# Optimization experiments

Hardware: AMD Instinct MI355X
Metric: run time of the kernel (lower is better)

## Reference

```python
import jax, jax.numpy as jnp
import numpy as np
from jax import lax

B, HS, WS, C, NH, WIN = 32, 56, 56, 192, 6, 7
HID = int(C * 4.0)
EPS = 1e-5


def _ln(x, g, b):
    m = jnp.mean(x, -1, keepdims=True)
    v = jnp.mean((x - m) ** 2, -1, keepdims=True)
    return (x - m) * jax.lax.rsqrt(v + EPS) * g + b


def _cpe(x, H, W, w, b):
    # x: [B, H*W, C]; depthwise 3x3 conv positional encoding, residual add
    Bn = x.shape[0]
    feat = x.reshape(Bn, H, W, C).transpose(0, 3, 1, 2)  # NCHW
    out = lax.conv_general_dilated(feat, w, (1, 1), 'SAME',
                                   feature_group_count=C,
                                   dimension_numbers=('NCHW', 'OIHW', 'NCHW'))
    out = out + b[None, :, None, None]
    pos = out.transpose(0, 2, 3, 1).reshape(Bn, H * W, C)
    return x + pos


def _window_attn(xw, qkv_w, qkv_b, proj_w, proj_b):
    # xw: [nW, N, C]; faithful einops split 'b n (d k h) -> k b h n d'
    nW, N, _ = xw.shape
    hd = C // NH
    qkv = xw @ qkv_w + qkv_b                      # [nW, N, 3C]
    qkv = qkv.reshape(nW, N, hd, 3, NH)           # (d k h) split
    q, k, v = jnp.moveaxis(qkv.transpose(3, 0, 4, 1, 2), 0, 0)  # each [nW, NH, N, hd]
    scale = hd ** -0.5
    scores = jnp.einsum('bhid,bhjd->bhij', q, k) * scale
    attn = jax.nn.softmax(scores, axis=-1)
    out = jnp.einsum('bhij,bhjd->bhid', attn, v)  # [nW, NH, N, hd]
    out = out.transpose(0, 2, 1, 3).reshape(nW, N, C)  # 'b h n d -> b n (h d)'
    return out @ proj_w + proj_b


def _forward(x, H, W, cpe0_w, cpe0_b, cpe1_w, cpe1_b, n1_g, n1_b,
             qkv_w, qkv_b, proj_w, proj_b, n2_g, n2_b,
             fc1_w, fc1_b, fc2_w, fc2_b):
    Bn = x.shape[0]
    shortcut = _cpe(x, H, W, cpe0_w, cpe0_b)
    y = _ln(shortcut, n1_g, n1_b).reshape(Bn, H, W, C)
    pad_r = (WIN - W % WIN) % WIN
    pad_b = (WIN - H % WIN) % WIN
    y = jnp.pad(y, ((0, 0), (0, pad_b), (0, pad_r), (0, 0)))
    Hp, Wp = H + pad_b, W + pad_r
    nh, nw = Hp // WIN, Wp // WIN
    # faithful: 'b (w_h nw_h) (w_w nw_w) c -> (b nw_h nw_w) (w_h w_w) c'
    y = y.reshape(Bn, WIN, nh, WIN, nw, C).transpose(0, 2, 4, 1, 3, 5)
    y = y.reshape(Bn * nh * nw, WIN * WIN, C)
    y = _window_attn(y, qkv_w, qkv_b, proj_w, proj_b)
    # reverse: '(b nw_h nw_w) (w_h w_w) c -> b (w_h nw_h) (w_w nw_w) c'
    y = y.reshape(Bn, nh, nw, WIN, WIN, C).transpose(0, 3, 1, 4, 2, 5)
    y = y.reshape(Bn, Hp, Wp, C)[:, :H, :W, :].reshape(Bn, H * W, C)
    y = shortcut + y
    y = _cpe(y, H, W, cpe1_w, cpe1_b)
    h = _ln(y, n2_g, n2_b)
    h = jax.nn.gelu(h @ fc1_w + fc1_b, approximate=False) @ fc2_w + fc2_b
    return y + h


def setup_inputs() -> dict:
    key = jax.random.key(0)
    ks = jax.random.split(key, 12)
    s = 0.02
    return {
        'x': jax.random.normal(ks[0], (B, HS * WS, C), jnp.float32),
        'H': HS, 'W': WS,
        'cpe0_w': jax.random.normal(ks[1], (C, 1, 3, 3), jnp.float32) * s,
        'cpe0_b': jnp.zeros((C,), jnp.float32),
        'cpe1_w': jax.random.normal(ks[2], (C, 1, 3, 3), jnp.float32) * s,
        'cpe1_b': jnp.zeros((C,), jnp.float32),
        'n1_g': jnp.ones((C,), jnp.float32), 'n1_b': jnp.zeros((C,), jnp.float32),
        'qkv_w': jax.random.normal(ks[3], (C, 3 * C), jnp.float32) * s,
        'qkv_b': jnp.zeros((3 * C,), jnp.float32),
        'proj_w': jax.random.normal(ks[4], (C, C), jnp.float32) * s,
        'proj_b': jnp.zeros((C,), jnp.float32),
        'n2_g': jnp.ones((C,), jnp.float32), 'n2_b': jnp.zeros((C,), jnp.float32),
        'fc1_w': jax.random.normal(ks[5], (C, HID), jnp.float32) * s,
        'fc1_b': jnp.zeros((HID,), jnp.float32),
        'fc2_w': jax.random.normal(ks[6], (HID, C), jnp.float32) * s,
        'fc2_b': jnp.zeros((C,), jnp.float32),
    }


def reference(x, H, W, cpe0_w, cpe0_b, cpe1_w, cpe1_b, n1_g, n1_b,
              qkv_w, qkv_b, proj_w, proj_b, n2_g, n2_b,
              fc1_w, fc1_b, fc2_w, fc2_b):
    return _forward(x, H, W, cpe0_w, cpe0_b, cpe1_w, cpe1_b, n1_g, n1_b,
                    qkv_w, qkv_b, proj_w, proj_b, n2_g, n2_b,
                    fc1_w, fc1_b, fc2_w, fc2_b)
```

## Files before the change

kernel.cpp:

```cpp
#include <hip/hip_runtime.h>
#include <hip/hip_bf16.h>
#include <math.h>

#define Bn   32
#define Hh   56
#define Wd   56
#define Cc   192
#define NHh  6
#define HDim 32
#define HIDN 768
#define Tt   (Bn*Hh*Wd)
#define NWIN (Bn*64)

typedef __attribute__((ext_vector_type(8))) short short8;
typedef __attribute__((ext_vector_type(4))) short s4v;
typedef __attribute__((ext_vector_type(4))) float floatx4;

__device__ __forceinline__ short f2bf(float f) {
    unsigned u = __float_as_uint(f);
    u += 0x7fffu + ((u >> 16) & 1u);
    return (short)(u >> 16);
}
__device__ __forceinline__ float bf2f(short s) {
    return __uint_as_float(((unsigned)(unsigned short)s) << 16);
}

__device__ __forceinline__ int xcd_swz(int bid, int nb) {
    return (bid & 7) * (nb >> 3) + (bid >> 3);
}

__global__ void k_transpose(const float* __restrict__ W, short* __restrict__ WT,
                            int K, int N) {
    int idx = blockIdx.x * 256 + threadIdx.x;
    if (idx >= K * N) return;
    int n = idx / K, k = idx % K;
    WT[idx] = f2bf(W[k * N + n]);
}

__global__ void k_transpose_qkv(const float* __restrict__ W, short* __restrict__ WT) {
    int idx = blockIdx.x * 256 + threadIdx.x;
    if (idx >= 192 * 576) return;
    int n = idx / 192, kk = idx % 192;
    int d = n & 31, hh = (n >> 5) % 6, k3 = n / 192;
    int oc = d * 18 + k3 * 6 + hh;
    WT[idx] = f2bf(W[kk * 576 + oc]);
}

__global__ void __launch_bounds__(256) k_cpe_ln(
    const float* __restrict__ xin, const float* __restrict__ wconv,
    const float* __restrict__ bconv, const float* __restrict__ g,
    const float* __restrict__ beta, float* __restrict__ ysum_out,
    short* __restrict__ ln_out, int windowed)
{
    const int lane = threadIdx.x & 63;
    const int wv   = threadIdx.x >> 6;
    const bool act = lane < 48;
    const int c4   = (lane < 48 ? lane : lane - 16) * 4;

    const floatx4 zf = {0.f, 0.f, 0.f, 0.f};
    float wreg[36];
    #pragma unroll
    for (int i = 0; i < 9; ++i)
        *(floatx4*)&wreg[i * 4] = *(const floatx4*)(wconv + c4 * 9 + i * 4);
    const floatx4 gv  = *(const floatx4*)(g + c4);
    const floatx4 bv  = *(const floatx4*)(beta + c4);
    const floatx4 bcv = *(const floatx4*)(bconv + c4);

    const int W = xcd_swz(blockIdx.x, gridDim.x) * 4 + wv;
    const int b = W / (Hh * 7);
    const int rem = W % (Hh * 7);
    const int h = rem / 7, wslot = rem % 7;
    const int w0 = wslot * 8;

    floatx4 r[3][10];
    const int hy0 = (h > 0) ? h - 1 : 0;
    const int hy2 = (h < Hh - 1) ? h + 1 : Hh - 1;
    const int hys[3] = {hy0, h, hy2};
    #pragma unroll
    for (int dy = 0; dy < 3; ++dy) {
        const float* rp = xin + ((size_t)b * (Hh * Wd) + hys[dy] * Wd) * Cc + c4;
        #pragma unroll
        for (int j = 0; j < 10; ++j) {
            int wx = w0 - 1 + j;
            int wc = (wx < 0) ? 0 : ((wx > Wd - 1) ? Wd - 1 : wx);
            r[dy][j] = *(const floatx4*)(rp + wc * Cc);
        }
    }
    if (h == 0) {
        #pragma unroll
        for (int j = 0; j < 10; ++j) r[0][j] = zf;
    }
    if (h == Hh - 1) {
        #pragma unroll
        for (int j = 0; j < 10; ++j) r[2][j] = zf;
    }
    if (w0 == 0)      { r[0][0] = zf; r[1][0] = zf; r[2][0] = zf; }
    if (w0 == Wd - 8) { r[0][9] = zf; r[1][9] = zf; r[2][9] = zf; }

    floatx4 val[8];
    #pragma unroll
    for (int tk = 0; tk < 8; ++tk) {
        floatx4 a = bcv;
        #pragma unroll
        for (int dy = 0; dy < 3; ++dy) {
            #pragma unroll
            for (int dx = 0; dx < 3; ++dx) {
                const int t = dy * 3 + dx;
                floatx4 v = r[dy][tk + dx];
                #pragma unroll
                for (int j = 0; j < 4; ++j)
                    a[j] += wreg[j * 9 + t] * v[j];
            }
        }
        floatx4 xc = r[1][tk + 1];
        #pragma unroll
        for (int j = 0; j < 4; ++j) val[tk][j] = xc[j] + a[j];
    }

    float s[8], s2[8];
    #pragma unroll
    for (int tk = 0; tk < 8; ++tk) {
        float a = val[tk][0] + val[tk][1] + val[tk][2] + val[tk][3];
        float a2 = val[tk][0]*val[tk][0] + val[tk][1]*val[tk][1]
                 + val[tk][2]*val[tk][2] + val[tk][3]*val[tk][3];
        s[tk]  = act ? a  : 0.f;
        s2[tk] = act ? a2 : 0.f;
    }
    #pragma unroll
    for (int off = 1; off < 64; off <<= 1) {
        #pragma unroll
        for (int tk = 0; tk < 8; ++tk) {
            s[tk]  += __shfl_xor(s[tk],  off, 64);
            s2[tk] += __shfl_xor(s2[tk], off, 64);
        }
    }

    const int blk0 = (b * Hh + h) * Wd + w0;
    #pragma unroll
    for (int tk = 0; tk < 8; ++tk) {
        const float mean = s[tk] * (1.0f / Cc);
        const float var  = s2[tk] * (1.0f / Cc) - mean * mean;
        const float rs   = rsqrtf(var + 1e-5f);
        int rr;
        if (windowed) {
            int win = b * 64 + (h & 7) * 8 + tk;
            int pos = (h >> 3) * 7 + wslot;
            rr = win * 49 + pos;
        } else {
            rr = blk0 + tk;
        }
        if (act) {
            *(floatx4*)(ysum_out + (size_t)(blk0 + tk) * Cc + c4) = val[tk];
            s4v o;
            #pragma unroll
            for (int j = 0; j < 4; ++j)
                o[j] = f2bf((val[tk][j] - mean) * rs * gv[j] + bv[j]);
            *(s4v*)(ln_out + (size_t)rr * Cc + c4) = o;
        }
    }
}

template<int K, int EPI>
__global__ void __launch_bounds__(256) k_gemm_tiled(
    const short* __restrict__ A, const short* __restrict__ BT,
    const float* __restrict__ bias, void* __restrict__ outp)
{
    __shared__ __align__(16) short As[128 * 32];
    __shared__ __align__(16) short Bs[64 * 32];
    const int tid = threadIdx.x;
    const int gx = gridDim.x;
    const int flat = blockIdx.y * gx + blockIdx.x;
    const int swz = xcd_swz(flat, gx * gridDim.y);
    const int n0 = (swz % gx) * 64;
    const int m0 = (swz / gx) * 128;
    const int w = tid >> 6, lane = tid & 63;
    const int lcol = lane & 15, quad = lane >> 4;

    floatx4 acc[2][4];
    #pragma unroll
    for (int mi = 0; mi < 2; ++mi)
        #pragma unroll
        for (int ni = 0; ni < 4; ++ni) acc[mi][ni] = (floatx4){0, 0, 0, 0};

    const int ar = tid >> 2, ac = (tid & 3) * 8;
    const short* agp  = A + (size_t)(m0 + ar) * K + ac;
    const short* agp2 = A + (size_t)(m0 + 64 + ar) * K + ac;
    const short* bgp  = BT + (size_t)(n0 + ar) * K + ac;
    short* asw = As + tid * 8;
    short* bsw = Bs + tid * 8;

    const short* ard0 = As + (w * 32 + lcol) * 32 + quad * 8;
    const short* ard1 = As + (w * 32 + 16 + lcol) * 32 + quad * 8;
    const short* brd  = Bs + lcol * 32 + quad * 8;

    for (int k0 = 0; k0 < K; k0 += 32) {
        __syncthreads();
        short8 va0 = *(const short8*)(agp + k0);
        short8 va1 = *(const short8*)(agp2 + k0);
        short8 vb  = *(const short8*)(bgp + k0);
        *(short8*)asw             = va0;
        *(short8*)(asw + 64 * 32) = va1;
        *(short8*)bsw             = vb;
        __syncthreads();
        short8 a0 = *(const short8*)ard0;
        short8 a1 = *(const short8*)ard1;
        #pragma unroll
        for (int ni = 0; ni < 4; ++ni) {
            short8 b = *(const short8*)(brd + ni * 16 * 32);
            acc[0][ni] = __builtin_amdgcn_mfma_f32_16x16x32_bf16(a0, b, acc[0][ni], 0, 0, 0);
            acc[1][ni] = __builtin_amdgcn_mfma_f32_16x16x32_bf16(a1, b, acc[1][ni], 0, 0, 0);
        }
    }

    #pragma unroll
    for (int mi = 0; mi < 2; ++mi) {
        #pragma unroll
        for (int ni = 0; ni < 4; ++ni) {
            int col = n0 + ni * 16 + lcol;
            float bv;
            if (EPI == 0) {
                int d = col & 31, hh = (col >> 5) % 6, k3 = col / 192;
                bv = bias[d * 18 + k3 * 6 + hh];
            } else {
                bv = bias[col];
            }
            #pragma unroll
            for (int t = 0; t < 4; ++t) {
                int row = m0 + w * 32 + mi * 16 + quad * 4 + t;
                float v = acc[mi][ni][t] + bv;
                if (EPI == 0) {
                    ((short*)outp)[(size_t)row * 576 + col] = f2bf(v);
                } else if (EPI == 1) {
                    int win = row / 49, p = row % 49;
                    int b = win >> 6, wm = (win >> 3) & 7, wwm = win & 7;
                    int hh = (p / 7) * 8 + wm, ww = (p % 7) * 8 + wwm;
                    ((float*)outp)[((size_t)b * (Hh * Wd) + hh * Wd + ww) * Cc + col] += v;
                } else if (EPI == 2) {
                    float gl = 0.5f * v * (1.0f + erff(v * 0.70710678118654752f));
                    ((short*)outp)[(size_t)row * HIDN + col] = f2bf(gl);
                } else {
                    ((float*)outp)[(size_t)row * Cc + col] += v;
                }
            }
        }
    }
}

__global__ void __launch_bounds__(64) k_attn(
    const short* __restrict__ C, short* __restrict__ aout)
{
    int h = blockIdx.x, win = blockIdx.y;
    int lane = threadIdx.x;
    int lcol = lane & 15, quad = lane >> 4;
    __shared__ __align__(16) short buf[7424];
    short* Q  = buf;
    short* Kb = buf + 2560;
    short* Vt = buf + 5120;
    short* P  = buf;

    const short8 z8 = {0, 0, 0, 0, 0, 0, 0, 0};
    const size_t wbase = (size_t)win * 49 * 576;
    const int hq = h * 32;
    const int pr = lane >> 2, d8 = (lane & 3) * 8;

    #pragma unroll
    for (int it = 0; it < 4; ++it) {
        int pp = pr + it * 16;
        bool ok = pp < 49;
        size_t ro = wbase + (size_t)(ok ? pp : 0) * 576 + hq + d8;
        short8 vq = ok ? *(const short8*)(C + ro)       : z8;
        short8 vk = ok ? *(const short8*)(C + ro + 192) : z8;
        *(short8*)(Q  + pp * 40 + d8) = vq;
        *(short8*)(Kb + pp * 40 + d8) = vk;
    }
    #pragma unroll
    for (int it = 0; it < 4; ++it) {
        int pp = pr + it * 16;
        bool ok = pp < 49;
        size_t ro = wbase + (size_t)(ok ? pp : 0) * 576 + 384 + hq + d8;
        short8 vv = ok ? *(const short8*)(C + ro) : z8;
        #pragma unroll
        for (int j = 0; j < 8; ++j)
            Vt[(d8 + j) * 72 + pp] = vv[j];
    }

    floatx4 s[4][4];
    #pragma unroll
    for (int mi = 0; mi < 4; ++mi) {
        short8 aq = *(const short8*)(Q + (mi * 16 + lcol) * 40 + quad * 8);
        #pragma unroll
        for (int ni = 0; ni < 4; ++ni) {
            short8 bk = *(const short8*)(Kb + (ni * 16 + lcol) * 40 + quad * 8);
            floatx4 z = {0, 0, 0, 0};
            s[mi][ni] = __builtin_amdgcn_mfma_f32_16x16x32_bf16(aq, bk, z, 0, 0, 0);
        }
    }

    const float scale = 0.17677669529663688f;
    #pragma unroll
    for (int mi = 0; mi < 4; ++mi) {
        #pragma unroll
        for (int reg = 0; reg < 4; ++reg) {
            float vv[4];
            float mx = -3e38f;
            #pragma unroll
            for (int ni = 0; ni < 4; ++ni) {
                int col = ni * 16 + lcol;
                float v = (col < 49) ? s[mi][ni][reg] * scale : -3e38f;
                vv[ni] = v;
                mx = fmaxf(mx, v);
            }
            #pragma unroll
            for (int off = 1; off < 16; off <<= 1)
                mx = fmaxf(mx, __shfl_xor(mx, off, 64));
            float sum = 0.f;
            #pragma unroll
            for (int ni = 0; ni < 4; ++ni) {
                int col = ni * 16 + lcol;
                float e = (col < 49) ? __expf(vv[ni] - mx) : 0.f;
                vv[ni] = e;
                sum += e;
            }
            #pragma unroll
            for (int off = 1; off < 16; off <<= 1)
                sum += __shfl_xor(sum, off, 64);
            float inv = 1.0f / sum;
            int row = mi * 16 + quad * 4 + reg;
            #pragma unroll
            for (int ni = 0; ni < 4; ++ni)
                P[row * 72 + ni * 16 + lcol] = f2bf(vv[ni] * inv);
        }
    }

    #pragma unroll
    for (int mi = 0; mi < 4; ++mi) {
        short8 a0 = *(const short8*)(P + (mi * 16 + lcol) * 72 + quad * 8);
        short8 a1 = *(const short8*)(P + (mi * 16 + lcol) * 72 + 32 + quad * 8);
        #pragma unroll
        for (int nd = 0; nd < 2; ++nd) {
            short8 b0 = *(const short8*)(Vt + (nd * 16 + lcol) * 72 + quad * 8);
            short8 b1 = *(const short8*)(Vt + (nd * 16 + lcol) * 72 + 32 + quad * 8);
            floatx4 z = {0, 0, 0, 0};
            floatx4 o = __builtin_amdgcn_mfma_f32_16x16x32_bf16(a0, b0, z, 0, 0, 0);
            o = __builtin_amdgcn_mfma_f32_16x16x32_bf16(a1, b1, o, 0, 0, 0);
            #pragma unroll
            for (int reg = 0; reg < 4; ++reg) {
                int row = mi * 16 + quad * 4 + reg;
                if (row < 49)
                    aout[((size_t)win * 49 + row) * Cc + h * HDim + nd * 16 + lcol] =
                        f2bf(o[reg]);
            }
        }
    }
}

extern "C" void kernel_launch(void* const* d_in, const int* in_sizes, int n_in,
                              void* d_out, int out_size, void* d_ws, size_t ws_size,
                              hipStream_t stream)
{
    (void)in_sizes; (void)n_in; (void)out_size; (void)ws_size;
    const float* x      = (const float*)d_in[0];
    const float* cpe0_w = (const float*)d_in[3];
    const float* cpe0_b = (const float*)d_in[4];
    const float* cpe1_w = (const float*)d_in[5];
    const float* cpe1_b = (const float*)d_in[6];
    const float* n1_g   = (const float*)d_in[7];
    const float* n1_b   = (const float*)d_in[8];
    const float* qkv_w  = (const float*)d_in[9];
    const float* qkv_b  = (const float*)d_in[10];
    const float* proj_w = (const float*)d_in[11];
    const float* proj_b = (const float*)d_in[12];
    const float* n2_g   = (const float*)d_in[13];
    const float* n2_b   = (const float*)d_in[14];
    const float* fc1_w  = (const float*)d_in[15];
    const float* fc1_b  = (const float*)d_in[16];
    const float* fc2_w  = (const float*)d_in[17];
    const float* fc2_b  = (const float*)d_in[18];
    float* out = (float*)d_out;

    char* ws = (char*)d_ws;
    float* shortcut = (float*)ws;
    short* lnbuf    = (short*)(ws + 77070336);
    short* qkvbuf   = (short*)(ws + 115605504);
    short* attnout  = (short*)(ws + 231211008);
    short* h1       = qkvbuf;
    short* wqkvT    = (short*)(ws + 269746176);
    short* wprojT   = (short*)(ws + 269967360);
    short* wfc1T    = (short*)(ws + 270041088);
    short* wfc2T    = (short*)(ws + 270336000);

    k_transpose_qkv<<<dim3((192 * 576 + 255) / 256), dim3(256), 0, stream>>>(qkv_w, wqkvT);
    k_transpose<<<dim3((192 * 192 + 255) / 256), dim3(256), 0, stream>>>(proj_w, wprojT, 192, 192);
    k_transpose<<<dim3((192 * 768 + 255) / 256), dim3(256), 0, stream>>>(fc1_w, wfc1T, 192, 768);
    k_transpose<<<dim3((768 * 192 + 255) / 256), dim3(256), 0, stream>>>(fc2_w, wfc2T, 768, 192);

    k_cpe_ln<<<dim3(Tt / 32), dim3(256), 0, stream>>>(x, cpe0_w, cpe0_b, n1_g, n1_b,
                                                      shortcut, lnbuf, 1);
    k_gemm_tiled<192, 0><<<dim3(9, Tt / 128), dim3(256), 0, stream>>>(lnbuf, wqkvT, qkv_b, qkvbuf);
    k_attn<<<dim3(NHh, NWIN), dim3(64), 0, stream>>>(qkvbuf, attnout);
    k_gemm_tiled<192, 1><<<dim3(3, Tt / 128), dim3(256), 0, stream>>>(attnout, wprojT, proj_b, shortcut);
    k_cpe_ln<<<dim3(Tt / 32), dim3(256), 0, stream>>>(shortcut, cpe1_w, cpe1_b, n2_g, n2_b,
                                                      out, lnbuf, 0);
    k_gemm_tiled<192, 2><<<dim3(12, Tt / 128), dim3(256), 0, stream>>>(lnbuf, wfc1T, fc1_b, h1);
    k_gemm_tiled<768, 3><<<dim3(3, Tt / 128), dim3(256), 0, stream>>>(h1, wfc2T, fc2_b, out);
}
```

Measured before the change: 599.0 us.

## Fuse MLP fc1+GELU+fc2 into one kernel keeping hidden activations in LDS

Replaces the two separate MLP GEMM launches with one kernel. Each block handles 32 tokens: it computes fc1 with GELU into a bf16 hidden tile held in shared memory, then runs fc2 from that tile and adds the result into the output. This removes the global-memory round trip of the 768-wide hidden activation and one launch. In exchange, weight operands are read straight from global memory per wave with small M tiles (32 rows), so weight reuse drops, and the large LDS footprint limits occupancy.

```diff
diff --git a/kernel.cpp b/kernel.cpp
--- a/kernel.cpp
+++ b/kernel.cpp
@@ -230,19 +230,120 @@
                 float v = acc[mi][ni][t] + bv;
                 if (EPI == 0) {
                     ((short*)outp)[(size_t)row * 576 + col] = f2bf(v);
-                } else if (EPI == 1) {
+                } else {
                     int win = row / 49, p = row % 49;
                     int b = win >> 6, wm = (win >> 3) & 7, wwm = win & 7;
                     int hh = (p / 7) * 8 + wm, ww = (p % 7) * 8 + wwm;
                     ((float*)outp)[((size_t)b * (Hh * Wd) + hh * Wd + ww) * Cc + col] += v;
-                } else if (EPI == 2) {
+                }
+            }
+        }
+    }
+}
+
+__global__ void __launch_bounds__(256, 2) k_mlp(
+    const short* __restrict__ A,
+    const short* __restrict__ W1T,
+    const float* __restrict__ b1,
+    const short* __restrict__ W2T,
+    const float* __restrict__ b2,
+    float* __restrict__ out)
+{
+    __shared__ __align__(16) char lds[74752];
+    short (*As)[200] = (short (*)[200])lds;
+    float (*Cs)[196] = (float (*)[196])lds;
+    short (*Hs)[776] = (short (*)[776])(lds + 25088);
+
+    const int tid = threadIdx.x;
+    const int m0 = xcd_swz(blockIdx.x, gridDim.x) * 32;
+    const int wv = tid >> 6, lane = tid & 63;
+    const int lcol = lane & 15, quad = lane >> 4;
+
+    for (int i = tid; i < 32 * 24; i += 256) {
+        int r = i / 24, c = (i % 24) * 8;
+        *(short8*)&As[r][c] = *(const short8*)(A + (size_t)(m0 + r) * 192 + c);
+    }
+    __syncthreads();
+
+    #pragma unroll
+    for (int pass = 0; pass < 3; ++pass) {
+        const int n0 = wv * 192 + pass * 64;
+        floatx4 acc[4][2];
+        #pragma unroll
+        for (int mi = 0; mi < 4; ++mi) {
+            #pragma unroll
+            for (int nt = 0; nt < 2; ++nt) acc[mi][nt] = (floatx4){0, 0, 0, 0};
+        }
+        #pragma unroll
+        for (int k0 = 0; k0 < 192; k0 += 32) {
+            short8 bt0 = *(const short8*)&As[lcol][k0 + quad * 8];
+            short8 bt1 = *(const short8*)&As[16 + lcol][k0 + quad * 8];
+            #pragma unroll
+            for (int mi = 0; mi < 4; ++mi) {
+                short8 a = *(const short8*)(W1T + (size_t)(n0 + mi * 16 + lcol) * 192
+                                            + k0 + quad * 8);
+                acc[mi][0] = __builtin_amdgcn_mfma_f32_16x16x32_bf16(a, bt0, acc[mi][0], 0, 0, 0);
+                acc[mi][1] = __builtin_amdgcn_mfma_f32_16x16x32_bf16(a, bt1, acc[mi][1], 0, 0, 0);
+            }
+        }
+        #pragma unroll
+        for (int mi = 0; mi < 4; ++mi) {
+            const int hbase = n0 + mi * 16 + quad * 4;
+            floatx4 b1v = *(const floatx4*)(b1 + hbase);
+            #pragma unroll
+            for (int nt = 0; nt < 2; ++nt) {
+                s4v o;
+                #pragma unroll
+                for (int reg = 0; reg < 4; ++reg) {
+                    float v = acc[mi][nt][reg] + b1v[reg];
                     float gl = 0.5f * v * (1.0f + erff(v * 0.70710678118654752f));
-                    ((short*)outp)[(size_t)row * HIDN + col] = f2bf(gl);
-                } else {
-                    ((float*)outp)[(size_t)row * Cc + col] += v;
+                    o[reg] = f2bf(gl);
                 }
-            }
-        }
+                *(s4v*)&Hs[nt * 16 + lcol][hbase] = o;
+            }
+        }
+    }
+    __syncthreads();
+
+    const int c0 = wv * 48;
+    floatx4 acc2[3][2];
+    #pragma unroll
+    for (int mi = 0; mi < 3; ++mi) {
+        #pragma unroll
+        for (int nt = 0; nt < 2; ++nt) acc2[mi][nt] = (floatx4){0, 0, 0, 0};
+    }
+    #pragma unroll 4
+    for (int k0 = 0; k0 < 768; k0 += 32) {
+        short8 bt0 = *(const short8*)&Hs[lcol][k0 + quad * 8];
+        short8 bt1 = *(const short8*)&Hs[16 + lcol][k0 + quad * 8];
+        #pragma unroll
+        for (int mi = 0; mi < 3; ++mi) {
+            short8 a = *(const short8*)(W2T + (size_t)(c0 + mi * 16 + lcol) * 768
+                                        + k0 + quad * 8);
+            acc2[mi][0] = __builtin_amdgcn_mfma_f32_16x16x32_bf16(a, bt0, acc2[mi][0], 0, 0, 0);
+            acc2[mi][1] = __builtin_amdgcn_mfma_f32_16x16x32_bf16(a, bt1, acc2[mi][1], 0, 0, 0);
+        }
+    }
+    #pragma unroll
+    for (int mi = 0; mi < 3; ++mi) {
+        const int cbase = c0 + mi * 16 + quad * 4;
+        floatx4 b2v = *(const floatx4*)(b2 + cbase);
+        #pragma unroll
+        for (int nt = 0; nt < 2; ++nt) {
+            #pragma unroll
+            for (int reg = 0; reg < 4; ++reg)
+                Cs[nt * 16 + lcol][cbase + reg] = acc2[mi][nt][reg] + b2v[reg];
+        }
+    }
+    __syncthreads();
+    for (int i = tid; i < 32 * 48; i += 256) {
+        int t = i / 48, c = (i % 48) * 4;
+        floatx4* po = (floatx4*)(out + (size_t)(m0 + t) * 192 + c);
+        floatx4 cv = *(floatx4*)&Cs[t][c];
+        floatx4 ov = *po;
+        #pragma unroll
+        for (int j = 0; j < 4; ++j) ov[j] += cv[j];
+        *po = ov;
     }
 }
 
@@ -383,7 +484,6 @@
     short* lnbuf    = (short*)(ws + 77070336);
     short* qkvbuf   = (short*)(ws + 115605504);
     short* attnout  = (short*)(ws + 231211008);
-    short* h1       = qkvbuf;
     short* wqkvT    = (short*)(ws + 269746176);
     short* wprojT   = (short*)(ws + 269967360);
     short* wfc1T    = (short*)(ws + 270041088);
@@ -401,6 +501,5 @@
     k_gemm_tiled<192, 1><<<dim3(3, Tt / 128), dim3(256), 0, stream>>>(attnout, wprojT, proj_b, shortcut);
     k_cpe_ln<<<dim3(Tt / 32), dim3(256), 0, stream>>>(shortcut, cpe1_w, cpe1_b, n2_g, n2_b,
                                                       out, lnbuf, 0);
-    k_gemm_tiled<192, 2><<<dim3(12, Tt / 128), dim3(256), 0, stream>>>(lnbuf, wfc1T, fc1_b, h1);
-    k_gemm_tiled<768, 3><<<dim3(3, Tt / 128), dim3(256), 0, stream>>>(h1, wfc2T, fc2_b, out);
-}
+    k_mlp<<<dim3(Tt / 32), dim3(256), 0, stream>>>(lnbuf, wfc1T, fc1_b, wfc2T, fc2_b, out);
+}
```

Measured after the change: 731.5 us. 22.1% more time.

## Fuse window-reverse residual add into second CPE kernel and prefetch GEMM tiles

Applied to the files above, without the earlier changes.

The proj GEMM now writes bf16 output in window order to a scratch buffer, replacing the scattered fp32 read-modify-write into the shortcut. The second CPE+LN kernel adds that projection back, gathering window-ordered rows as it loads its 3x3 neighbourhood. Separately, the tiled GEMM prefetches the next K slice into registers before computing on the current one, so global loads overlap the MFMA work. The cost is about nine redundant bf16 proj loads per input element in the conv halo, plus some precision loss because the projection is stored in bf16 before the residual add.

```diff
diff --git a/kernel.cpp b/kernel.cpp
--- a/kernel.cpp
+++ b/kernel.cpp
@@ -46,11 +46,12 @@
     WT[idx] = f2bf(W[kk * 576 + oc]);
 }
 
+template<int ADDP>
 __global__ void __launch_bounds__(256) k_cpe_ln(
     const float* __restrict__ xin, const float* __restrict__ wconv,
     const float* __restrict__ bconv, const float* __restrict__ g,
     const float* __restrict__ beta, float* __restrict__ ysum_out,
-    short* __restrict__ ln_out, int windowed)
+    short* __restrict__ ln_out, int windowed, const short* __restrict__ proj)
 {
     const int lane = threadIdx.x & 63;
     const int wv   = threadIdx.x >> 6;
@@ -78,12 +79,21 @@
     const int hys[3] = {hy0, h, hy2};
     #pragma unroll
     for (int dy = 0; dy < 3; ++dy) {
-        const float* rp = xin + ((size_t)b * (Hh * Wd) + hys[dy] * Wd) * Cc + c4;
+        const int hy = hys[dy];
+        const float* rp = xin + ((size_t)b * (Hh * Wd) + hy * Wd) * Cc + c4;
         #pragma unroll
         for (int j = 0; j < 10; ++j) {
             int wx = w0 - 1 + j;
             int wc = (wx < 0) ? 0 : ((wx > Wd - 1) ? Wd - 1 : wx);
-            r[dy][j] = *(const floatx4*)(rp + wc * Cc);
+            floatx4 v = *(const floatx4*)(rp + wc * Cc);
+            if (ADDP) {
+                int prow = (b * 64 + (hy & 7) * 8 + (wc & 7)) * 49
+                         + (hy >> 3) * 7 + (wc >> 3);
+                s4v pv = *(const s4v*)(proj + (size_t)prow * Cc + c4);
+                #pragma unroll
+                for (int q = 0; q < 4; ++q) v[q] += bf2f(pv[q]);
+            }
+            r[dy][j] = v;
         }
     }
     if (h == 0) {
@@ -193,15 +203,21 @@
     const short* ard1 = As + (w * 32 + 16 + lcol) * 32 + quad * 8;
     const short* brd  = Bs + lcol * 32 + quad * 8;
 
+    short8 va0 = *(const short8*)(agp);
+    short8 va1 = *(const short8*)(agp2);
+    short8 vb  = *(const short8*)(bgp);
+
     for (int k0 = 0; k0 < K; k0 += 32) {
         __syncthreads();
-        short8 va0 = *(const short8*)(agp + k0);
-        short8 va1 = *(const short8*)(agp2 + k0);
-        short8 vb  = *(const short8*)(bgp + k0);
         *(short8*)asw             = va0;
         *(short8*)(asw + 64 * 32) = va1;
         *(short8*)bsw             = vb;
         __syncthreads();
+        if (k0 + 32 < K) {
+            va0 = *(const short8*)(agp + k0 + 32);
+            va1 = *(const short8*)(agp2 + k0 + 32);
+            vb  = *(const short8*)(bgp + k0 + 32);
+        }
         short8 a0 = *(const short8*)ard0;
         short8 a1 = *(const short8*)ard1;
         #pragma unroll
@@ -230,16 +246,13 @@
                 float v = acc[mi][ni][t] + bv;
                 if (EPI == 0) {
                     ((short*)outp)[(size_t)row * 576 + col] = f2bf(v);
-                } else if (EPI == 1) {
-                    int win = row / 49, p = row % 49;
-                    int b = win >> 6, wm = (win >> 3) & 7, wwm = win & 7;
-                    int hh = (p / 7) * 8 + wm, ww = (p % 7) * 8 + wwm;
-                    ((float*)outp)[((size_t)b * (Hh * Wd) + hh * Wd + ww) * Cc + col] += v;
                 } else if (EPI == 2) {
                     float gl = 0.5f * v * (1.0f + erff(v * 0.70710678118654752f));
                     ((short*)outp)[(size_t)row * HIDN + col] = f2bf(gl);
+                } else if (EPI == 3) {
+                    ((float*)outp)[(size_t)row * Cc + col] += v;
                 } else {
-                    ((float*)outp)[(size_t)row * Cc + col] += v;
+                    ((short*)outp)[(size_t)row * Cc + col] = f2bf(v);
                 }
             }
         }
@@ -383,6 +396,7 @@
     short* lnbuf    = (short*)(ws + 77070336);
     short* qkvbuf   = (short*)(ws + 115605504);
     short* attnout  = (short*)(ws + 231211008);
+    short* projbuf  = qkvbuf;
     short* h1       = qkvbuf;
     short* wqkvT    = (short*)(ws + 269746176);
     short* wprojT   = (short*)(ws + 269967360);
@@ -394,13 +408,13 @@
     k_transpose<<<dim3((192 * 768 + 255) / 256), dim3(256), 0, stream>>>(fc1_w, wfc1T, 192, 768);
     k_transpose<<<dim3((768 * 192 + 255) / 256), dim3(256), 0, stream>>>(fc2_w, wfc2T, 768, 192);
 
-    k_cpe_ln<<<dim3(Tt / 32), dim3(256), 0, stream>>>(x, cpe0_w, cpe0_b, n1_g, n1_b,
-                                                      shortcut, lnbuf, 1);
+    k_cpe_ln<0><<<dim3(Tt / 32), dim3(256), 0, stream>>>(x, cpe0_w, cpe0_b, n1_g, n1_b,
+                                                         shortcut, lnbuf, 1, nullptr);
     k_gemm_tiled<192, 0><<<dim3(9, Tt / 128), dim3(256), 0, stream>>>(lnbuf, wqkvT, qkv_b, qkvbuf);
     k_attn<<<dim3(NHh, NWIN), dim3(64), 0, stream>>>(qkvbuf, attnout);
-    k_gemm_tiled<192, 1><<<dim3(3, Tt / 128), dim3(256), 0, stream>>>(attnout, wprojT, proj_b, shortcut);
-    k_cpe_ln<<<dim3(Tt / 32), dim3(256), 0, stream>>>(shortcut, cpe1_w, cpe1_b, n2_g, n2_b,
-                                                      out, lnbuf, 0);
+    k_gemm_tiled<192, 4><<<dim3(3, Tt / 128), dim3(256), 0, stream>>>(attnout, wprojT, proj_b, projbuf);
+    k_cpe_ln<1><<<dim3(Tt / 32), dim3(256), 0, stream>>>(shortcut, cpe1_w, cpe1_b, n2_g, n2_b,
+                                                         out, lnbuf, 0, projbuf);
     k_gemm_tiled<192, 2><<<dim3(12, Tt / 128), dim3(256), 0, stream>>>(lnbuf, wfc1T, fc1_b, h1);
     k_gemm_tiled<768, 3><<<dim3(3, Tt / 128), dim3(256), 0, stream>>>(h1, wfc2T, fc2_b, out);
 }
```

Result: faster. 557.4 us (-6.9%).
